# Optimization experiments

Measured on AMD Instinct MI355X. Metric: run time of the kernel, lower is better.

The kernel has to match this reference:

```python
import jax, jax.numpy as jnp
import numpy as np

B, RES, DIM, H, KD = 16, 32, 768, 12, 64
N = RES * RES          # 1024 tokens
D = KD                 # attn_ratio = 1 -> per-head value dim == key_dim
DH = D * H             # 768
SCALE = KD ** -0.5
LN_EPS = 1e-5


def _bias_idxs():
    # replicate the itertools.product construction: for row-major points,
    # offsets (|dy|,|dx|) are first seen in order dy-major, so id = |dy|*RES + |dx|
    coords = np.arange(N)
    y, x = coords // RES, coords % RES
    dy = np.abs(y[:, None] - y[None, :])
    dx = np.abs(x[:, None] - x[None, :])
    return jnp.asarray(dy * RES + dx, dtype=jnp.int32)  # [N, N]


def setup_inputs() -> dict:
    key = jax.random.key(0)
    ks = jax.random.split(key, 8)
    return {
        "x": jax.random.normal(ks[0], (B, N, DIM), jnp.float32),
        "ln_w": 1.0 + 0.01 * jax.random.normal(ks[1], (DIM,), jnp.float32),
        "ln_b": 0.01 * jax.random.normal(ks[2], (DIM,), jnp.float32),
        "qkv_w": 0.02 * jax.random.normal(ks[3], (3 * H * KD, DIM), jnp.float32),
        "qkv_b": 0.01 * jax.random.normal(ks[4], (3 * H * KD,), jnp.float32),
        "proj_w": 0.02 * jax.random.normal(ks[5], (DIM, DH), jnp.float32),
        "proj_b": 0.01 * jax.random.normal(ks[6], (DIM,), jnp.float32),
        "attn_biases": 0.1 * jax.random.normal(ks[7], (H, RES * RES), jnp.float32),
        "bias_idxs": _bias_idxs(),
    }


def reference(x, ln_w, ln_b, qkv_w, qkv_b, proj_w, proj_b, attn_biases, bias_idxs):
    # LayerNorm over the feature dim
    mu = jnp.mean(x, axis=-1, keepdims=True)
    var = jnp.mean(jnp.square(x - mu), axis=-1, keepdims=True)
    xn = (x - mu) * jax.lax.rsqrt(var + LN_EPS) * ln_w + ln_b

    # fused qkv projection -> [B, N, H, 3*KD], split per head
    qkv = (xn @ qkv_w.T + qkv_b).reshape(B, N, H, 3 * KD)
    q, k, v = jnp.split(qkv, [KD, 2 * KD], axis=3)  # each [B, N, H, KD]

    # gathered relative-position bias: [H, N, N]
    bias = attn_biases[:, bias_idxs]

    # scores + bias -> softmax -> AV
    attn = jnp.einsum("bnhk,bmhk->bhnm", q, k) * SCALE + bias[None]
    attn = jax.nn.softmax(attn, axis=-1)
    out = jnp.einsum("bhnm,bmhd->bnhd", attn, v).reshape(B, N, DH)
    return out @ proj_w.T + proj_b
```

## Files before the change

kernel.cpp:

```cpp
#include <hip/hip_runtime.h>
#include <cstdint>
#include <cstddef>

#define AS1 __attribute__((address_space(1)))
#define AS3 __attribute__((address_space(3)))

typedef float f32x4 __attribute__((ext_vector_type(4)));
typedef __bf16 bf16x8 __attribute__((ext_vector_type(8)));
typedef __bf16 bf16x4 __attribute__((ext_vector_type(4)));
typedef uint32_t u32x4 __attribute__((ext_vector_type(4)));

__device__ __forceinline__ void async_cp16(void* lds, const void* g) {
    __builtin_amdgcn_global_load_lds((AS1 void*)(g), (AS3 void*)(lds), 16, 0, 0);
}

__device__ __forceinline__ bf16x8 frag_of(u32x4 u) {
    return __builtin_bit_cast(bf16x8, u);
}

__global__ __launch_bounds__(256)
void fused_pre(const float* __restrict__ qkvw, const float* __restrict__ projw,
               __bf16* __restrict__ qkvwb, __bf16* __restrict__ projwb,
               const float* __restrict__ x, const float* __restrict__ w,
               const float* __restrict__ bsh, __bf16* __restrict__ xn) {
    if (blockIdx.x < 2304) {
        int i = blockIdx.x * 256 + threadIdx.x;
        if (i < 442368) {
            int row = i / 192, c4 = (i - row * 192) * 4;
            int t = (row >= 1536) ? 2 : (row >= 768 ? 1 : 0);
            int rem = row - t * 768;
            int hh = rem >> 6, d = rem & 63;
            int in_row = hh * 192 + t * 64 + d;
            float4 v = *(const float4*)(qkvw + (long)in_row * 768 + c4);
            bf16x4 o;
            o[0] = (__bf16)v.x; o[1] = (__bf16)v.y; o[2] = (__bf16)v.z; o[3] = (__bf16)v.w;
            *(bf16x4*)(qkvwb + (long)row * 768 + c4) = o;
        } else {
            int j = i - 442368;
            float4 v = ((const float4*)projw)[j];
            bf16x4 o;
            o[0] = (__bf16)v.x; o[1] = (__bf16)v.y; o[2] = (__bf16)v.z; o[3] = (__bf16)v.w;
            ((bf16x4*)projwb)[j] = o;
        }
        return;
    }
    const int lane = threadIdx.x & 63;
    const long row = (long)(blockIdx.x - 2304) * 4 + (threadIdx.x >> 6);
    const float4* xr = (const float4*)(x + row * 768);
    float4 v[3];
    v[0] = xr[lane]; v[1] = xr[lane + 64]; v[2] = xr[lane + 128];
    float s = 0.f, ss = 0.f;
#pragma unroll
    for (int i = 0; i < 3; ++i) {
        s  += v[i].x + v[i].y + v[i].z + v[i].w;
        ss += v[i].x * v[i].x + v[i].y * v[i].y + v[i].z * v[i].z + v[i].w * v[i].w;
    }
#pragma unroll
    for (int m = 1; m < 64; m <<= 1) { s += __shfl_xor(s, m); ss += __shfl_xor(ss, m); }
    const float mean = s * (1.f / 768.f);
    const float rstd = rsqrtf(ss * (1.f / 768.f) - mean * mean + 1e-5f);
    const float4* wv = (const float4*)w;
    const float4* bv = (const float4*)bsh;
    bf16x4* outp = (bf16x4*)(xn + row * 768);
#pragma unroll
    for (int i = 0; i < 3; ++i) {
        float4 wi = wv[lane + 64 * i], bi = bv[lane + 64 * i];
        bf16x4 o;
        o[0] = (__bf16)((v[i].x - mean) * rstd * wi.x + bi.x);
        o[1] = (__bf16)((v[i].y - mean) * rstd * wi.y + bi.y);
        o[2] = (__bf16)((v[i].z - mean) * rstd * wi.z + bi.z);
        o[3] = (__bf16)((v[i].w - mean) * rstd * wi.w + bi.w);
        outp[lane + 64 * i] = o;
    }
}

template <int MODE>
__device__ __forceinline__
void gemm_core(char* smem,
               const __bf16* __restrict__ A, const __bf16* __restrict__ Bw,
               const float* __restrict__ bias,
               __bf16* __restrict__ q_out, __bf16* __restrict__ k_out,
               __bf16* __restrict__ vt_out, float* __restrict__ f_out,
               long bm, long bn) {
    constexpr int K = 768;
    const int tid  = threadIdx.x;
    const int lane = tid & 63;
    const int quad = lane >> 4;
    const int l16  = lane & 15;
    const int wave = tid >> 6;
    const int wm = wave >> 1, wn = wave & 1;

    const __bf16* Ab = A  + bm * K;
    const __bf16* Bb = Bw + bn * K;

    const int e0 = tid, e1 = tid + 256;
    const int rA0 = e0 >> 2, c0 = ((e0 & 3) ^ ((e0 >> 3) & 3)) * 8;
    const int rA1 = e1 >> 2, c1 = ((e1 & 3) ^ ((e1 >> 3) & 3)) * 8;
    const int swq = quad ^ ((l16 >> 1) & 3);

    f32x4 acc[4][4] = {};

    auto stage = [&](int t) {
        char* base = smem + (t % 3) * 16384;
        const __bf16* As_ = Ab + t * 32;
        const __bf16* Bs_ = Bb + t * 32;
        async_cp16(base + e0 * 16,        As_ + (long)rA0 * K + c0);
        async_cp16(base + e1 * 16,        As_ + (long)rA1 * K + c1);
        async_cp16(base + 8192 + e0 * 16, Bs_ + (long)rA0 * K + c0);
        async_cp16(base + 8192 + e1 * 16, Bs_ + (long)rA1 * K + c1);
    };

    auto kstep = [&](int buf) {
        const u32x4* Av = (const u32x4*)(smem + buf * 16384);
        const u32x4* Bv = (const u32x4*)(smem + buf * 16384 + 8192);
        bf16x8 af[4], bfr[4];
#pragma unroll
        for (int t = 0; t < 4; ++t) {
            af[t]  = frag_of(Av[(wm * 64 + t * 16 + l16) * 4 + swq]);
            bfr[t] = frag_of(Bv[(wn * 64 + t * 16 + l16) * 4 + swq]);
        }
        __builtin_amdgcn_s_setprio(1);
#pragma unroll
        for (int i = 0; i < 4; ++i)
#pragma unroll
            for (int j = 0; j < 4; ++j) {
                if constexpr (MODE == 0)
                    acc[i][j] = __builtin_amdgcn_mfma_f32_16x16x32_bf16(bfr[j], af[i], acc[i][j], 0, 0, 0);
                else
                    acc[i][j] = __builtin_amdgcn_mfma_f32_16x16x32_bf16(af[i], bfr[j], acc[i][j], 0, 0, 0);
            }
        __builtin_amdgcn_s_setprio(0);
    };

    stage(0); stage(1);
    for (int t = 0; t < 23; ++t) {
        asm volatile("s_waitcnt vmcnt(4)" ::: "memory");
        __builtin_amdgcn_s_barrier();
        if (t < 22) stage(t + 2);
        kstep(t % 3);
    }
    asm volatile("s_waitcnt vmcnt(0)" ::: "memory");
    __builtin_amdgcn_s_barrier();
    kstep(23 % 3);

    if constexpr (MODE == 0) {
#pragma unroll
        for (int j = 0; j < 4; ++j) {
            int col0 = (int)bn + wn * 64 + j * 16 + quad * 4;
            int t  = col0 >= 768;
            int cc = col0 - t * 768;
            int h  = cc >> 6, d = cc & 63;
            int f  = h * 192 + t * 64 + d;
            float4 bb = *(const float4*)(bias + f);
            __bf16* dst = t ? k_out : q_out;
#pragma unroll
            for (int i = 0; i < 4; ++i) {
                long row = bm + wm * 64 + i * 16 + l16;
                long b   = row >> 10;
                long n   = row & 1023;
                bf16x4 pk;
                pk[0] = (__bf16)(acc[i][j][0] + bb.x);
                pk[1] = (__bf16)(acc[i][j][1] + bb.y);
                pk[2] = (__bf16)(acc[i][j][2] + bb.z);
                pk[3] = (__bf16)(acc[i][j][3] + bb.w);
                *(bf16x4*)(dst + ((b * 12 + h) * 1024 + n) * 64 + d) = pk;
            }
        }
    } else if constexpr (MODE == 2) {
#pragma unroll
        for (int j = 0; j < 4; ++j) {
            int cv = (int)bn - 1536 + wn * 64 + j * 16 + l16;
            int h  = cv >> 6, d = cv & 63;
            float bv = bias[h * 192 + 128 + d];
#pragma unroll
            for (int i = 0; i < 4; ++i) {
                long row0 = bm + wm * 64 + i * 16 + quad * 4;
                long b    = row0 >> 10;
                long n0   = row0 & 1023;
                bf16x4 pk;
                pk[0] = (__bf16)(acc[i][j][0] + bv);
                pk[1] = (__bf16)(acc[i][j][1] + bv);
                pk[2] = (__bf16)(acc[i][j][2] + bv);
                pk[3] = (__bf16)(acc[i][j][3] + bv);
                *(bf16x4*)(vt_out + ((b * 12 + h) * 64 + d) * 1024 + n0) = pk;
            }
        }
    } else {
#pragma unroll
        for (int i = 0; i < 4; ++i) {
#pragma unroll
            for (int r = 0; r < 4; ++r) {
                long row = bm + wm * 64 + i * 16 + quad * 4 + r;
#pragma unroll
                for (int j = 0; j < 4; ++j) {
                    int col = (int)bn + wn * 64 + j * 16 + l16;
                    f_out[row * 768 + col] = acc[i][j][r] + bias[col];
                }
            }
        }
    }
}

__global__ __launch_bounds__(256, 3)
void gemm_qkv(const __bf16* __restrict__ A, const __bf16* __restrict__ Bw,
              const float* __restrict__ bias, __bf16* __restrict__ qb,
              __bf16* __restrict__ kb, __bf16* __restrict__ vtb) {
    __shared__ __align__(16) char smem[49152];
    int blk  = blockIdx.x;
    int xcd  = blk & 7;
    int rest = blk >> 3;
    int bx   = rest % 18;
    int byg  = rest / 18;
    long by  = xcd + 8 * byg;
    if (bx < 12)
        gemm_core<0>(smem, A, Bw, bias, qb, kb, nullptr, nullptr, by * 128, (long)bx * 128);
    else
        gemm_core<2>(smem, A, Bw, bias, nullptr, nullptr, vtb, nullptr, by * 128, (long)bx * 128);
}

__global__ __launch_bounds__(256, 3)
void gemm_proj(const __bf16* __restrict__ A, const __bf16* __restrict__ Bw,
               const float* __restrict__ bias, float* __restrict__ out) {
    __shared__ __align__(16) char smem[49152];
    int blk  = blockIdx.x;
    int xcd  = blk & 7;
    int rest = blk >> 3;
    int bx   = rest % 6;
    int byg  = rest / 6;
    long by  = xcd + 8 * byg;
    gemm_core<1>(smem, A, Bw, bias, nullptr, nullptr, nullptr, out,
                 by * 128, (long)bx * 128);
}

__global__ __launch_bounds__(256, 5)
void attn_kernel(const __bf16* __restrict__ Q, const __bf16* __restrict__ Kb,
                 const __bf16* __restrict__ Vt, const float* __restrict__ biases,
                 __bf16* __restrict__ out) {
    __shared__ __align__(16) char smem[28672];
    float* brow = (float*)(smem + 24576);

    const int tid  = threadIdx.x;
    const int lane = tid & 63;
    const int wave = tid >> 6;
    const int quad = lane >> 4;
    const int l16  = lane & 15;
    const int sw   = l16 & 7;
    const int swp  = (l16 >> 1) & 3;

    int blk  = blockIdx.x;
    int xcd  = blk & 7;
    int rest = blk >> 3;
    int qt   = rest & 7;
    int bhg  = rest >> 3;
    int bh_i = xcd + 8 * bhg;
    int b    = bh_i / 12;
    int h    = bh_i - b * 12;

    const long bh = bh_i;
    const __bf16* Qg  = Q  + (bh * 1024 + qt * 128) * 64;
    const __bf16* Kg  = Kb + bh * 1024 * 64;
    const __bf16* Vtg = Vt + bh * 64 * 1024;

    const int rk = tid >> 3;
    const int ck = (tid & 7) ^ (rk & 7);
    const int rv = tid >> 2;
    const int cv = (tid & 3) ^ ((tid >> 3) & 3);

    {
        const float LOG2E = 1.4426950408889634f;
        float4 v = ((const float4*)(biases + (long)h * 1024))[tid];
        float4 o; o.x = v.x * LOG2E; o.y = v.y * LOG2E;
        o.z = v.z * LOG2E; o.w = v.w * LOG2E;
        ((float4*)brow)[tid] = o;
    }
#pragma unroll
    for (int j = 0; j < 4; ++j) {
        int e = tid + 256 * j;
        int r = e >> 3, c = (e & 7) ^ (r & 7);
        async_cp16(smem + e * 16, Qg + r * 64 + c * 8);
    }
    __syncthreads();

    bf16x8 aq[2][2];
    {
        const u32x4* Qv = (const u32x4*)smem;
#pragma unroll
        for (int g = 0; g < 2; ++g) {
            int qrow = wave * 32 + g * 16 + l16;
            aq[g][0] = frag_of(Qv[qrow * 8 + (quad ^ sw)]);
            aq[g][1] = frag_of(Qv[qrow * 8 + ((quad + 4) ^ sw)]);
        }
    }
    __syncthreads();
    async_cp16(smem + tid * 16,        Kg  + rk * 64   + ck * 8);
    async_cp16(smem + 8192 + tid * 16, Vtg + rv * 1024 + cv * 8);
    __syncthreads();

    const int yq = 4 * qt + wave;
    int pdx00[4], pdx01[4], pdx10[4];
#pragma unroll
    for (int r = 0; r < 4; ++r) {
        int d0 = l16 - (quad * 4 + r);
        pdx00[r] = d0 < 0 ? -d0 : d0;
        pdx01[r] = 16 - d0;
        pdx10[r] = 16 + d0;
    }

    const float SSCALE = 0.125f * 1.4426950408889634f;
    float lacc[2] = {0.f, 0.f};
    f32x4 o[2][4] = {};
    char* Pw = smem + 16384 + wave * 2048;
    const int hb = (quad & 1) * 8;
    const int pslotw = (quad >> 1);

    for (int kt = 0; kt < 32; ++kt) {
        const int cb = kt & 1;
        if (kt < 31) {
            const int nb = cb ^ 1;
            async_cp16(smem + nb * 4096 + tid * 16,
                       Kg + (kt + 1) * 2048 + rk * 64 + ck * 8);
            async_cp16(smem + 8192 + nb * 4096 + tid * 16,
                       Vtg + (kt + 1) * 32 + rv * 1024 + cv * 8);
            asm volatile("s_waitcnt vmcnt(2)" ::: "memory");
        } else {
            asm volatile("s_waitcnt vmcnt(0)" ::: "memory");
        }
        __builtin_amdgcn_sched_barrier(0);
        __builtin_amdgcn_s_barrier();

        f32x4 s[2][2];
        const u32x4* Kv = (const u32x4*)(smem + cb * 4096);
#pragma unroll
        for (int nt = 0; nt < 2; ++nt) {
            int krow = nt * 16 + l16;
            bf16x8 k0 = frag_of(Kv[krow * 8 + (quad ^ sw)]);
            bf16x8 k1 = frag_of(Kv[krow * 8 + ((quad + 4) ^ sw)]);
#pragma unroll
            for (int g = 0; g < 2; ++g) {
                f32x4 z = {0.f, 0.f, 0.f, 0.f};
                z = __builtin_amdgcn_mfma_f32_16x16x32_bf16(k0, aq[g][0], z, 0, 0, 0);
                z = __builtin_amdgcn_mfma_f32_16x16x32_bf16(k1, aq[g][1], z, 0, 0, 0);
                s[g][nt] = z;
            }
        }

        int dyv = yq - kt; dyv = dyv < 0 ? -dyv : dyv;
        const float* br = brow + dyv * 32;
#pragma unroll
        for (int g = 0; g < 2; ++g) {
#pragma unroll
            for (int nt = 0; nt < 2; ++nt) {
                const int* pdx = (g == nt) ? pdx00 : (g ? pdx10 : pdx01);
                bf16x4 pk;
#pragma unroll
                for (int r = 0; r < 4; ++r) {
                    float p = __builtin_amdgcn_exp2f(s[g][nt][r] * SSCALE + br[pdx[r]]);
                    lacc[g] += p;
                    pk[r] = (__bf16)p;
                }
                int slot = (nt * 2 + pslotw) ^ swp;
                *(bf16x4*)(Pw + (g * 16 + l16) * 64 + slot * 16 + hb) = pk;
            }
        }

        bf16x8 bp[2];
#pragma unroll
        for (int g = 0; g < 2; ++g)
            bp[g] = frag_of(*(const u32x4*)(Pw + (g * 16 + l16) * 64 + ((quad ^ swp) << 4)));
        const char* Vb = smem + 8192 + cb * 4096;
#pragma unroll
        for (int dt = 0; dt < 4; ++dt) {
            bf16x8 vf = frag_of(*(const u32x4*)(Vb + (dt * 16 + l16) * 64 + ((quad ^ swp) << 4)));
#pragma unroll
            for (int g = 0; g < 2; ++g)
                o[g][dt] = __builtin_amdgcn_mfma_f32_16x16x32_bf16(vf, bp[g], o[g][dt], 0, 0, 0);
        }

        asm volatile("s_waitcnt lgkmcnt(0)" ::: "memory");
        __builtin_amdgcn_sched_barrier(0);
        __builtin_amdgcn_s_barrier();
    }

#pragma unroll
    for (int g = 0; g < 2; ++g) {
        float la = lacc[g];
        la += __shfl_xor(la, 16);
        la += __shfl_xor(la, 32);
        const float rl = 1.f / la;
        const long n = qt * 128 + wave * 32 + g * 16 + l16;
        __bf16* op = out + ((long)b * 1024 + n) * 768 + h * 64 + quad * 4;
#pragma unroll
        for (int dt = 0; dt < 4; ++dt) {
            bf16x4 ov;
            ov[0] = (__bf16)(o[g][dt][0] * rl);
            ov[1] = (__bf16)(o[g][dt][1] * rl);
            ov[2] = (__bf16)(o[g][dt][2] * rl);
            ov[3] = (__bf16)(o[g][dt][3] * rl);
            *(bf16x4*)(op + dt * 16) = ov;
        }
    }
}

extern "C" void kernel_launch(void* const* d_in, const int* in_sizes, int n_in,
                              void* d_out, int out_size, void* d_ws, size_t ws_size,
                              hipStream_t stream) {
    (void)in_sizes; (void)n_in; (void)out_size; (void)ws_size;
    const float* x      = (const float*)d_in[0];
    const float* ln_w   = (const float*)d_in[1];
    const float* ln_b   = (const float*)d_in[2];
    const float* qkv_w  = (const float*)d_in[3];
    const float* qkv_b  = (const float*)d_in[4];
    const float* proj_w = (const float*)d_in[5];
    const float* proj_b = (const float*)d_in[6];
    const float* ab     = (const float*)d_in[7];
    float* outp = (float*)d_out;

    char* ws = (char*)d_ws;
    __bf16* xn     = (__bf16*)(ws);
    __bf16* aout   = (__bf16*)(ws);
    __bf16* qkvwb  = (__bf16*)(ws + 25165824);
    __bf16* projwb = (__bf16*)(ws + 28704768);
    __bf16* qb     = (__bf16*)(ws + 29884416);
    __bf16* kb     = (__bf16*)(ws + 55050240);
    __bf16* vtb    = (__bf16*)(ws + 80216064);

    fused_pre<<<6400, 256, 0, stream>>>(qkv_w, proj_w, qkvwb, projwb,
                                        x, ln_w, ln_b, xn);
    gemm_qkv<<<2304, 256, 0, stream>>>(xn, qkvwb, qkv_b, qb, kb, vtb);
    attn_kernel<<<1536, 256, 0, stream>>>(qb, kb, vtb, ab, aout);
    gemm_proj<<<768, 256, 0, stream>>>(aout, projwb, proj_b, outp);
}
```

Measured before the change: 326.0 us.

## Software-pipeline attention loop to overlap QK^T with previous tile's PV

Restructures the attention key-tile loop so each iteration computes scores for tile kt while doing the P·V product for tile kt-1. A prologue and epilogue handle the first and last tiles. V moves to triple-buffered LDS and LDS grows to 32 KB. The explicit vmcnt waits and split barriers become a single __syncthreads per iteration. The aim is to hide MFMA and softmax latency by interleaving independent work, at the cost of more LDS and a reliance on __syncthreads to order the async LDS loads.

```diff
diff --git a/kernel.cpp b/kernel.cpp
--- a/kernel.cpp
+++ b/kernel.cpp
@@ -236,8 +236,8 @@
 void attn_kernel(const __bf16* __restrict__ Q, const __bf16* __restrict__ Kb,
                  const __bf16* __restrict__ Vt, const float* __restrict__ biases,
                  __bf16* __restrict__ out) {
-    __shared__ __align__(16) char smem[28672];
-    float* brow = (float*)(smem + 24576);
+    __shared__ __align__(16) char smem[32768];
+    float* brow = (float*)(smem + 28672);
 
     const int tid  = threadIdx.x;
     const int lane = tid & 63;
@@ -309,27 +309,12 @@
     const float SSCALE = 0.125f * 1.4426950408889634f;
     float lacc[2] = {0.f, 0.f};
     f32x4 o[2][4] = {};
-    char* Pw = smem + 16384 + wave * 2048;
+    char* Pw = smem + 20480 + wave * 2048;
     const int hb = (quad & 1) * 8;
     const int pslotw = (quad >> 1);
 
-    for (int kt = 0; kt < 32; ++kt) {
-        const int cb = kt & 1;
-        if (kt < 31) {
-            const int nb = cb ^ 1;
-            async_cp16(smem + nb * 4096 + tid * 16,
-                       Kg + (kt + 1) * 2048 + rk * 64 + ck * 8);
-            async_cp16(smem + 8192 + nb * 4096 + tid * 16,
-                       Vtg + (kt + 1) * 32 + rv * 1024 + cv * 8);
-            asm volatile("s_waitcnt vmcnt(2)" ::: "memory");
-        } else {
-            asm volatile("s_waitcnt vmcnt(0)" ::: "memory");
-        }
-        __builtin_amdgcn_sched_barrier(0);
-        __builtin_amdgcn_s_barrier();
-
-        f32x4 s[2][2];
-        const u32x4* Kv = (const u32x4*)(smem + cb * 4096);
+    auto do_S = [&](int kt, f32x4 s[2][2]) {
+        const u32x4* Kv = (const u32x4*)(smem + (kt & 1) * 4096);
 #pragma unroll
         for (int nt = 0; nt < 2; ++nt) {
             int krow = nt * 16 + l16;
@@ -343,7 +328,22 @@
                 s[g][nt] = z;
             }
         }
-
+    };
+    auto do_PV = [&](int ktm1) {
+        bf16x8 bp[2];
+#pragma unroll
+        for (int g = 0; g < 2; ++g)
+            bp[g] = frag_of(*(const u32x4*)(Pw + (g * 16 + l16) * 64 + ((quad ^ swp) << 4)));
+        const char* Vb = smem + 8192 + (ktm1 % 3) * 4096;
+#pragma unroll
+        for (int dt = 0; dt < 4; ++dt) {
+            bf16x8 vf = frag_of(*(const u32x4*)(Vb + (dt * 16 + l16) * 64 + ((quad ^ swp) << 4)));
+#pragma unroll
+            for (int g = 0; g < 2; ++g)
+                o[g][dt] = __builtin_amdgcn_mfma_f32_16x16x32_bf16(vf, bp[g], o[g][dt], 0, 0, 0);
+        }
+    };
+    auto do_softmax = [&](int kt, f32x4 s[2][2]) {
         int dyv = yq - kt; dyv = dyv < 0 ? -dyv : dyv;
         const float* br = brow + dyv * 32;
 #pragma unroll
@@ -362,24 +362,30 @@
                 *(bf16x4*)(Pw + (g * 16 + l16) * 64 + slot * 16 + hb) = pk;
             }
         }
-
-        bf16x8 bp[2];
-#pragma unroll
-        for (int g = 0; g < 2; ++g)
-            bp[g] = frag_of(*(const u32x4*)(Pw + (g * 16 + l16) * 64 + ((quad ^ swp) << 4)));
-        const char* Vb = smem + 8192 + cb * 4096;
-#pragma unroll
-        for (int dt = 0; dt < 4; ++dt) {
-            bf16x8 vf = frag_of(*(const u32x4*)(Vb + (dt * 16 + l16) * 64 + ((quad ^ swp) << 4)));
-#pragma unroll
-            for (int g = 0; g < 2; ++g)
-                o[g][dt] = __builtin_amdgcn_mfma_f32_16x16x32_bf16(vf, bp[g], o[g][dt], 0, 0, 0);
-        }
-
-        asm volatile("s_waitcnt lgkmcnt(0)" ::: "memory");
-        __builtin_amdgcn_sched_barrier(0);
-        __builtin_amdgcn_s_barrier();
-    }
+    };
+    auto prefetch = [&](int ktn) {
+        async_cp16(smem + (ktn & 1) * 4096 + tid * 16,
+                   Kg + ktn * 2048 + rk * 64 + ck * 8);
+        async_cp16(smem + 8192 + (ktn % 3) * 4096 + tid * 16,
+                   Vtg + ktn * 32 + rv * 1024 + cv * 8);
+    };
+
+    {
+        prefetch(1);
+        f32x4 s[2][2];
+        do_S(0, s);
+        do_softmax(0, s);
+        __syncthreads();
+    }
+    for (int kt = 1; kt < 32; ++kt) {
+        if (kt < 31) prefetch(kt + 1);
+        f32x4 s[2][2];
+        do_S(kt, s);
+        do_PV(kt - 1);
+        do_softmax(kt, s);
+        __syncthreads();
+    }
+    do_PV(31);
 
 #pragma unroll
     for (int g = 0; g < 2; ++g) {
```

After: 335.8 us. +3.0%, slower.
